# Kernel optimization log

Hardware: AMD Instinct MI355X
Metric: run time of the kernel (lower is better)

The kernel has to match this reference:

```python
import jax, jax.numpy as jnp
import numpy as np

DIM = 1024
HEADS = 16
HIDDEN = 4 * DIM

def _gelu_erf(x):
    # GELU via erf, matching the torch module exactly
    return x * 0.5 * (1.0 + jax.lax.erf(x / jnp.sqrt(2.0).astype(x.dtype)))

def setup_inputs() -> dict:
    key = jax.random.key(0)
    ks = jax.random.split(key, 12)
    s = 0.02
    x = jax.random.normal(ks[0], (2, 2048, DIM), dtype=jnp.float32)
    # MHSA params
    ln1_g = jnp.ones((DIM,), jnp.float32)
    ln1_b = jnp.zeros((DIM,), jnp.float32)
    w_qkv = jax.random.normal(ks[1], (DIM, 3 * DIM), jnp.float32) * s  # no bias
    w_proj = jax.random.normal(ks[2], (DIM, DIM), jnp.float32) * s
    b_proj = jnp.zeros((DIM,), jnp.float32)
    # ResMLP params
    ln2_g = jnp.ones((DIM,), jnp.float32)
    ln2_b = jnp.zeros((DIM,), jnp.float32)
    w1 = jax.random.normal(ks[3], (DIM, HIDDEN), jnp.float32) * s
    b1 = jnp.zeros((HIDDEN,), jnp.float32)
    w2 = jax.random.normal(ks[4], (HIDDEN, DIM), jnp.float32) * s
    b2 = jnp.zeros((DIM,), jnp.float32)
    return {"x": x, "ln1_g": ln1_g, "ln1_b": ln1_b, "w_qkv": w_qkv,
            "w_proj": w_proj, "b_proj": b_proj, "ln2_g": ln2_g, "ln2_b": ln2_b,
            "w1": w1, "b1": b1, "w2": w2, "b2": b2}

def _layernorm(x, g, b, eps=1e-5):
    mu = jnp.mean(x, axis=-1, keepdims=True)
    var = jnp.mean(jnp.square(x - mu), axis=-1, keepdims=True)
    return (x - mu) * jax.lax.rsqrt(var + eps) * g + b

def reference(x, ln1_g, ln1_b, w_qkv, w_proj, b_proj, ln2_g, ln2_b, w1, b1, w2, b2):
    B, N, C = x.shape
    H = HEADS
    hd = C // H
    scale = hd ** -0.5
    # --- MHSA (dropout is identity in eval) ---
    h = _layernorm(x, ln1_g, ln1_b)
    qkv = (h @ w_qkv).reshape(B, N, 3, H, hd)
    q = jnp.transpose(qkv[:, :, 0], (0, 2, 1, 3))  # [B,H,N,hd]
    k = jnp.transpose(qkv[:, :, 1], (0, 2, 1, 3))
    v = jnp.transpose(qkv[:, :, 2], (0, 2, 1, 3))
    attn = jax.nn.softmax(jnp.einsum('bhnd,bhmd->bhnm', q, k) * scale, axis=-1)
    out = jnp.einsum('bhnm,bhmd->bhnd', attn, v)
    out = jnp.transpose(out, (0, 2, 1, 3)).reshape(B, N, C)
    x = x + out @ w_proj + b_proj
    # --- ResMLP ---
    h = _layernorm(x, ln2_g, ln2_b)
    h = _gelu_erf(h @ w1 + b1)
    x = x + h @ w2 + b2
    return x
```

## Files before the change

### kernel.cpp

```cpp
#include <hip/hip_runtime.h>
#include <stdint.h>


#define DIMC 1024
#define HIDN 4096
#define SEQ  2048
#define TOK  4096

typedef __bf16 bf16x8 __attribute__((ext_vector_type(8)));
typedef float  f32x4  __attribute__((ext_vector_type(4)));
typedef unsigned short ushort8 __attribute__((ext_vector_type(8)));

__device__ inline unsigned short f2bf(float f) {
  union { float f; unsigned u; } v; v.f = f;
  unsigned u = v.u;
  return (unsigned short)((u + 0x7fffu + ((u >> 16) & 1u)) >> 16);
}

__device__ inline unsigned cvt_pk_bf16(float a, float b) {
  unsigned r;
  asm("v_cvt_pk_bf16_f32 %0, %1, %2" : "=v"(r) : "v"(a), "v"(b));
  return r;
}

#if __has_builtin(__builtin_amdgcn_exp2f)
__device__ inline float fast_exp2(float x) { return __builtin_amdgcn_exp2f(x); }
#else
__device__ inline float fast_exp2(float x) { return exp2f(x); }
#endif

__device__ inline f32x4 mfma_bf16(bf16x8 a, bf16x8 b, f32x4 c) {
  return __builtin_amdgcn_mfma_f32_16x16x32_bf16(a, b, c, 0, 0, 0);
}

typedef const __attribute__((address_space(1))) unsigned int* as1_u32p;
typedef __attribute__((address_space(3))) unsigned int* as3_u32p;
__device__ inline void gload_lds16(const unsigned short* g, unsigned short* l) {
  __builtin_amdgcn_global_load_lds((as1_u32p)(const void*)g, (as3_u32p)(void*)l,
                                   16, 0, 0);
}

__global__ __launch_bounds__(256)
void prep_kernel(const float* __restrict__ wa, unsigned short* __restrict__ ta,
                 const float* __restrict__ wb, unsigned short* __restrict__ tb,
                 const float* __restrict__ wc, unsigned short* __restrict__ tc,
                 const float* __restrict__ wd, unsigned short* __restrict__ td,
                 const float* __restrict__ x, const float* __restrict__ g,
                 const float* __restrict__ bln, unsigned short* __restrict__ out) {
  const int bid = blockIdx.x;
  const int tid = threadIdx.x;
  if (bid < 12288) {
    __shared__ float tile[32][33];
    const float* w; unsigned short* wt; int K, N, bx, by;
    if (bid < 3072)      { w = wa; wt = ta; K = 1024; N = 3072; bx = bid % 96;  by = bid / 96; }
    else if (bid < 4096) { int i = bid - 3072; w = wb; wt = tb; K = 1024; N = 1024; bx = i % 32;  by = i / 32; }
    else if (bid < 8192) { int i = bid - 4096; w = wc; wt = tc; K = 1024; N = 4096; bx = i % 128; by = i / 128; }
    else                 { int i = bid - 8192; w = wd; wt = td; K = 4096; N = 1024; bx = i % 32;  by = i / 32; }
    const int k0 = by * 32;
    const int n0 = bx * 32;
    const int tx = tid & 31;
    const int ty = tid >> 5;
#pragma unroll
    for (int i = 0; i < 4; i++)
      tile[ty + i * 8][tx] = w[(size_t)(k0 + ty + i * 8) * N + n0 + tx];
    __syncthreads();
#pragma unroll
    for (int i = 0; i < 4; i++)
      wt[(size_t)(n0 + ty + i * 8) * K + k0 + tx] = f2bf(tile[tx][ty + i * 8]);
  } else {
    const int row = bid - 12288;
    const float4* xr = (const float4*)&x[(size_t)row * DIMC];
    float4 v = xr[tid];
    float s  = v.x + v.y + v.z + v.w;
    float sq = v.x * v.x + v.y * v.y + v.z * v.z + v.w * v.w;
#pragma unroll
    for (int off = 32; off > 0; off >>= 1) {
      s  += __shfl_xor(s, off, 64);
      sq += __shfl_xor(sq, off, 64);
    }
    __shared__ float red[8];
    if ((tid & 63) == 0) { red[tid >> 6] = s; red[4 + (tid >> 6)] = sq; }
    __syncthreads();
    s  = red[0] + red[1] + red[2] + red[3];
    sq = red[4] + red[5] + red[6] + red[7];
    const float mu  = s * (1.0f / DIMC);
    const float var = sq * (1.0f / DIMC) - mu * mu;
    const float rs  = rsqrtf(var + 1e-5f);
    const int c = tid * 4;
    float vv[4] = {v.x, v.y, v.z, v.w};
#pragma unroll
    for (int j = 0; j < 4; j++)
      out[(size_t)row * DIMC + c + j] = f2bf((vv[j] - mu) * rs * g[c + j] + bln[c + j]);
  }
}

__global__ __launch_bounds__(256)
void ln_kernel(const float* __restrict__ x, const float* __restrict__ g,
               const float* __restrict__ b, unsigned short* __restrict__ out) {
  const int row = blockIdx.x;
  const int tid = threadIdx.x;
  const float4* xr = (const float4*)&x[(size_t)row * DIMC];
  float4 v = xr[tid];
  float s  = v.x + v.y + v.z + v.w;
  float sq = v.x * v.x + v.y * v.y + v.z * v.z + v.w * v.w;
#pragma unroll
  for (int off = 32; off > 0; off >>= 1) {
    s  += __shfl_xor(s, off, 64);
    sq += __shfl_xor(sq, off, 64);
  }
  __shared__ float red[8];
  if ((tid & 63) == 0) { red[tid >> 6] = s; red[4 + (tid >> 6)] = sq; }
  __syncthreads();
  s  = red[0] + red[1] + red[2] + red[3];
  sq = red[4] + red[5] + red[6] + red[7];
  const float mu  = s * (1.0f / DIMC);
  const float var = sq * (1.0f / DIMC) - mu * mu;
  const float rs  = rsqrtf(var + 1e-5f);
  const int c = tid * 4;
  float vv[4] = {v.x, v.y, v.z, v.w};
#pragma unroll
  for (int j = 0; j < 4; j++)
    out[(size_t)row * DIMC + c + j] = f2bf((vv[j] - mu) * rs * g[c + j] + b[c + j]);
}

template <int EPI, int TN>
__global__ __launch_bounds__(256, (TN == 64) ? 4 : 3)
void gemm_bt(const unsigned short* __restrict__ A,
             const unsigned short* __restrict__ Bt,
             float* __restrict__ Cf, unsigned short* __restrict__ Cb,
             const float* __restrict__ bias, const float* __restrict__ res,
             int M, int N, int K,
             unsigned short* __restrict__ qd,
             unsigned short* __restrict__ kTd,
             unsigned short* __restrict__ vd) {
  constexpr int NU = TN / 32;
  constexpr int BP = TN / 32;
  __shared__ unsigned short As[128 * 64];
  __shared__ unsigned short Bs[TN * 64];
  const int gx  = N / TN;
  const int bid = blockIdx.x;
  const int xcd = bid & 7;
  const int lin = bid >> 3;
  const int bx  = lin % gx;
  const int by  = (xcd << 2) + lin / gx;
  const int tid  = threadIdx.x;
  const int lane = tid & 63;
  const int wave = tid >> 6;
  const int m0 = by * 128;
  const int n0 = bx * TN;
  const int wm = (wave >> 1) * 64;
  const int wn = (wave & 1) * (TN / 2);
  const int lm = lane & 15;
  const int lg = lane >> 4;
  const int r8 = tid >> 3;
  const int c8 = tid & 7;
  const int csrc = ((c8 ^ (r8 & 7)) * 8);

  const unsigned short* gA = &A [(size_t)(m0 + r8) * K + csrc];
  const unsigned short* gB = &Bt[(size_t)(n0 + r8) * K + csrc];

  f32x4 acc[4][NU];
#pragma unroll
  for (int t = 0; t < 4; t++)
#pragma unroll
    for (int u = 0; u < NU; u++) acc[t][u] = {0.f, 0.f, 0.f, 0.f};

  const int x0 = (lg ^ (lm & 7)) * 8;
  const int x1 = ((4 + lg) ^ (lm & 7)) * 8;

  for (int k0 = 0; k0 < K; k0 += 64) {
    __syncthreads();
#pragma unroll
    for (int p = 0; p < 4; p++)
      gload_lds16(gA + (size_t)p * 32 * K + k0, &As[p * 2048 + wave * 512]);
#pragma unroll
    for (int p = 0; p < BP; p++)
      gload_lds16(gB + (size_t)p * 32 * K + k0, &Bs[p * 2048 + wave * 512]);
    __syncthreads();
#pragma unroll
    for (int sub = 0; sub < 2; sub++) {
      const int xo = sub ? x1 : x0;
      bf16x8 af[4], bfr[NU];
#pragma unroll
      for (int t = 0; t < 4; t++)  af[t]  = *(const bf16x8*)&As[(wm + t * 16 + lm) * 64 + xo];
#pragma unroll
      for (int u = 0; u < NU; u++) bfr[u] = *(const bf16x8*)&Bs[(wn + u * 16 + lm) * 64 + xo];
#pragma unroll
      for (int t = 0; t < 4; t++)
#pragma unroll
        for (int u = 0; u < NU; u++)
          acc[t][u] = mfma_bf16(af[t], bfr[u], acc[t][u]);
    }
  }

#pragma unroll
  for (int t = 0; t < 4; t++) {
    const int row = m0 + wm + t * 16 + lg * 4;
#pragma unroll
    for (int u = 0; u < NU; u++) {
      const int col = n0 + wn + u * 16 + lm;
#pragma unroll
      for (int r = 0; r < 4; r++) {
        float v = acc[t][u][r];
        size_t idx = (size_t)(row + r) * N + col;
        if (EPI == 0) {
          const int rr = row + r;
          const int bb = rr >> 11, key = rr & (SEQ - 1);
          if (col < 1024) {
            qd[(size_t)rr * 1024 + col] = f2bf(v * 0.18033688011112042f);
          } else if (col < 2048) {
            const int d = col - 1024, h = d >> 6, dd = d & 63;
            kTd[(((size_t)(bb * 16 + h)) * SEQ + key) * 64 + dd] = f2bf(v);
          } else {
            vd[(size_t)rr * 1024 + (col - 2048)] = f2bf(v);
          }
        } else if (EPI == 1) {
          Cf[idx] = v + bias[col] + res[idx];
        } else {
          float xg = v + bias[col];
          Cb[idx] = f2bf(0.5f * xg * (1.0f + erff(xg * 0.70710678118654752f)));
        }
      }
    }
  }
}

__global__ __launch_bounds__(256)
void v_transpose(const unsigned short* __restrict__ vd,
                 unsigned short* __restrict__ vT) {
  const int kt = blockIdx.x;
  const int bh = blockIdx.y;
  const int b = bh >> 4, h = bh & 15;
  const int tid = threadIdx.x;
  __shared__ unsigned short tile[64 * 72];
  const int tok = tid >> 2;
  const int ch  = tid & 3;
  const size_t srow = (size_t)(b * SEQ + kt * 64 + tok) * 1024 + h * 64;
  ushort8 va = *(const ushort8*)&vd[srow + ch * 8];
  ushort8 vb = *(const ushort8*)&vd[srow + 32 + ch * 8];
  *(ushort8*)&tile[tok * 72 + ch * 8] = va;
  *(ushort8*)&tile[tok * 72 + 32 + ch * 8] = vb;
  __syncthreads();
  const int d = tid >> 2;
  ushort8 o0, o1;
#pragma unroll
  for (int j = 0; j < 8; j++) {
    o0[j] = tile[(ch * 8 + j) * 72 + d];
    o1[j] = tile[((ch + 4) * 8 + j) * 72 + d];
  }
  const size_t vdst = ((size_t)bh * 64 + d) * SEQ + kt * 64;
  *(ushort8*)&vT[vdst + ch * 8] = o0;
  *(ushort8*)&vT[vdst + 32 + ch * 8] = o1;
}

__global__ __launch_bounds__(256, 2)
void attn_kernel(const unsigned short* __restrict__ qbuf,
                 const unsigned short* __restrict__ kT,
                 const unsigned short* __restrict__ vT,
                 unsigned short* __restrict__ out) {
  const int bid = blockIdx.x;
  const int xcd = bid & 7;
  const int lin = bid >> 3;
  const int bh  = (xcd << 2) + (lin >> 4);
  const int qt  = lin & 15;
  const int b  = bh >> 4;
  const int h  = bh & 15;
  const int tid  = threadIdx.x;
  const int lane = tid & 63;
  const int wave = tid >> 6;
  const int ks   = wave >> 1;
  const int qh   = wave & 1;
  const int lm = lane & 15;
  const int lg = lane >> 4;

  __shared__ f32x4 shbuf[4096];
  unsigned short* Ks = (unsigned short*)shbuf;
  unsigned short* Vs = (unsigned short*)shbuf + 8192;
  unsigned short* Ps = (unsigned short*)shbuf + 16384;

  const int qrow_base = b * SEQ + qt * 128 + qh * 64;
  bf16x8 qb[4][2];
#pragma unroll
  for (int s = 0; s < 4; s++)
#pragma unroll
    for (int c = 0; c < 2; c++)
      qb[s][c] = *(const bf16x8*)&qbuf[(size_t)(qrow_base + s * 16 + lm) * 1024 +
                                       h * 64 + c * 32 + lg * 8];

  f32x4 o[4][4];
#pragma unroll
  for (int dt = 0; dt < 4; dt++)
#pragma unroll
    for (int s = 0; s < 4; s++) o[dt][s] = {0.f, 0.f, 0.f, 0.f};
  float li[4] = {0.f, 0.f, 0.f, 0.f};

  const unsigned short* kbp = &kT[(size_t)bh * SEQ * 64];
  const unsigned short* vbp = &vT[(size_t)bh * 64 * SEQ];
  const int ts   = tid & 127;
  const int srow = ts >> 3;
  const int slog = ((ts & 7) ^ (srow & 7)) * 8;
  const int koff = ks * 1024;
  const int xk0 = ((lg)     ^ (lm & 7)) * 8;
  const int xk1 = ((4 + lg) ^ (lm & 7)) * 8;
  unsigned short* ksb = Ks + ks * 4096;
  unsigned short* vsb = Vs + ks * 4096;
  unsigned short* psb = Ps + wave * 4096;
  unsigned short* kdst = ksb + ((ts >> 6) * 512);
  unsigned short* vdst = vsb + ((ts >> 6) * 512);

  for (int kt = 0; kt < 16; kt++) {
    __syncthreads();
#pragma unroll
    for (int p = 0; p < 4; p++) {
      gload_lds16(&kbp[(size_t)(koff + kt * 64 + p * 16 + srow) * 64 + slog],
                  kdst + p * 1024);
      gload_lds16(&vbp[(size_t)(p * 16 + srow) * SEQ + koff + kt * 64 + slog],
                  vdst + p * 1024);
    }
    __syncthreads();

#pragma unroll
    for (int u = 0; u < 4; u++) {
      bf16x8 ka0 = *(const bf16x8*)&ksb[(u * 16 + lm) * 64 + xk0];
      bf16x8 ka1 = *(const bf16x8*)&ksb[(u * 16 + lm) * 64 + xk1];
      f32x4 st[4];
#pragma unroll
      for (int s = 0; s < 4; s++) {
        f32x4 z = {0.f, 0.f, 0.f, 0.f};
        z = mfma_bf16(ka0, qb[s][0], z);
        z = mfma_bf16(ka1, qb[s][1], z);
        st[s] = z;
      }
#pragma unroll
      for (int s = 0; s < 4; s++) {
        float p0 = fast_exp2(st[s][0] - 8.0f);
        float p1 = fast_exp2(st[s][1] - 8.0f);
        float p2 = fast_exp2(st[s][2] - 8.0f);
        float p3 = fast_exp2(st[s][3] - 8.0f);
        li[s] += (p0 + p1) + (p2 + p3);
        uint2 pk;
        pk.x = cvt_pk_bf16(p0, p1);
        pk.y = cvt_pk_bf16(p2, p3);
        const int phys = (u * 2 + (lg >> 1)) ^ (lm & 7);
        *(uint2*)&psb[(s * 16 + lm) * 64 + phys * 8 + (lg & 1) * 4] = pk;
      }
    }

#pragma unroll
    for (int kc = 0; kc < 2; kc++) {
      const int xo = kc ? xk1 : xk0;
      bf16x8 pb[4];
#pragma unroll
      for (int s = 0; s < 4; s++)
        pb[s] = *(const bf16x8*)&psb[(s * 16 + lm) * 64 + xo];
#pragma unroll
      for (int dt = 0; dt < 4; dt++) {
        bf16x8 va = *(const bf16x8*)&vsb[(dt * 16 + lm) * 64 + xo];
#pragma unroll
        for (int s = 0; s < 4; s++)
          o[dt][s] = mfma_bf16(va, pb[s], o[dt][s]);
      }
    }
  }

  __syncthreads();
  f32x4* ob = shbuf + qh * 1088;
  float*  lb = (float*)(ob + 1024);
  if (ks == 1) {
#pragma unroll
    for (int dt = 0; dt < 4; dt++)
#pragma unroll
      for (int s = 0; s < 4; s++)
        ob[(dt * 4 + s) * 64 + lane] = o[dt][s];
#pragma unroll
    for (int s = 0; s < 4; s++) lb[s * 64 + lane] = li[s];
  }
  __syncthreads();
  if (ks == 0) {
#pragma unroll
    for (int dt = 0; dt < 4; dt++)
#pragma unroll
      for (int s = 0; s < 4; s++)
        o[dt][s] += ob[(dt * 4 + s) * 64 + lane];
#pragma unroll
    for (int s = 0; s < 4; s++) {
      float l = li[s] + lb[s * 64 + lane];
      l += __shfl_xor(l, 16, 64);
      l += __shfl_xor(l, 32, 64);
      const float inv = 1.0f / l;
#pragma unroll
      for (int dt = 0; dt < 4; dt++) {
        uint2 ok;
        ok.x = cvt_pk_bf16(o[dt][s][0] * inv, o[dt][s][1] * inv);
        ok.y = cvt_pk_bf16(o[dt][s][2] * inv, o[dt][s][3] * inv);
        *(uint2*)&out[(size_t)(qrow_base + s * 16 + lm) * DIMC + h * 64 +
                      dt * 16 + lg * 4] = ok;
      }
    }
  }
}

extern "C" void kernel_launch(void* const* d_in, const int* in_sizes, int n_in,
                              void* d_out, int out_size, void* d_ws, size_t ws_size,
                              hipStream_t stream) {
  const float* x      = (const float*)d_in[0];
  const float* ln1_g  = (const float*)d_in[1];
  const float* ln1_b  = (const float*)d_in[2];
  const float* w_qkv  = (const float*)d_in[3];
  const float* w_proj = (const float*)d_in[4];
  const float* b_proj = (const float*)d_in[5];
  const float* ln2_g  = (const float*)d_in[6];
  const float* ln2_b  = (const float*)d_in[7];
  const float* w1     = (const float*)d_in[8];
  const float* b1     = (const float*)d_in[9];
  const float* w2     = (const float*)d_in[10];
  const float* b2     = (const float*)d_in[11];
  float* out = (float*)d_out;

  char* ws = (char*)d_ws;
  size_t off = 0;
  auto alloc = [&](size_t bytes) { void* p = ws + off; off += (bytes + 255) & ~(size_t)255; return p; };
  unsigned short* wqkvT = (unsigned short*)alloc((size_t)3072 * 1024 * 2);
  unsigned short* wprjT = (unsigned short*)alloc((size_t)1024 * 1024 * 2);
  unsigned short* w1T   = (unsigned short*)alloc((size_t)4096 * 1024 * 2);
  unsigned short* w2T   = (unsigned short*)alloc((size_t)1024 * 4096 * 2);
  unsigned short* hb    = (unsigned short*)alloc((size_t)TOK * 1024 * 2);
  unsigned short* qbuf  = (unsigned short*)alloc((size_t)TOK * 1024 * 2);
  unsigned short* vdb   = (unsigned short*)alloc((size_t)TOK * 1024 * 2);
  unsigned short* attnb = (unsigned short*)alloc((size_t)TOK * 1024 * 2);
  float*          x1    = (float*)         alloc((size_t)TOK * 1024 * 4);
  unsigned short* hidb  = (unsigned short*)alloc((size_t)TOK * 4096 * 2);
  unsigned short* kT = hidb;
  unsigned short* vT = hidb + (size_t)32 * SEQ * 64;

  prep_kernel<<<12288 + TOK, 256, 0, stream>>>(w_qkv, wqkvT, w_proj, wprjT,
                                               w1, w1T, w2, w2T,
                                               x, ln1_g, ln1_b, hb);
  gemm_bt<0, 64><<<1536, 256, 0, stream>>>(
      hb, wqkvT, nullptr, nullptr, nullptr, nullptr, TOK, 3072, 1024,
      qbuf, kT, vdb);
  v_transpose<<<dim3(SEQ / 64, 32), 256, 0, stream>>>(vdb, vT);
  attn_kernel<<<512, 256, 0, stream>>>(qbuf, kT, vT, attnb);
  gemm_bt<1, 64><<<512, 256, 0, stream>>>(
      attnb, wprjT, x1, nullptr, b_proj, x, TOK, 1024, 1024,
      nullptr, nullptr, nullptr);
  ln_kernel<<<TOK, 256, 0, stream>>>(x1, ln2_g, ln2_b, hb);
  gemm_bt<2, 64><<<2048, 256, 0, stream>>>(
      hb, w1T, nullptr, hidb, b1, nullptr, TOK, 4096, 1024,
      nullptr, nullptr, nullptr);
  gemm_bt<1, 64><<<512, 256, 0, stream>>>(
      hidb, w2T, out, nullptr, b2, x1, TOK, 1024, 4096,
      nullptr, nullptr, nullptr);
}
```

Measured before the change: 339.6 us.

## Double-buffer LDS tiles in gemm_bt to overlap global loads with MFMA

```diff
diff --git a/kernel.cpp b/kernel.cpp
--- a/kernel.cpp
+++ b/kernel.cpp
@@ -124,7 +124,7 @@
 }
 
 template <int EPI, int TN>
-__global__ __launch_bounds__(256, (TN == 64) ? 4 : 3)
+__global__ __launch_bounds__(256, 3)
 void gemm_bt(const unsigned short* __restrict__ A,
              const unsigned short* __restrict__ Bt,
              float* __restrict__ Cf, unsigned short* __restrict__ Cb,
@@ -135,8 +135,10 @@
              unsigned short* __restrict__ vd) {
   constexpr int NU = TN / 32;
   constexpr int BP = TN / 32;
-  __shared__ unsigned short As[128 * 64];
-  __shared__ unsigned short Bs[TN * 64];
+  __shared__ unsigned short As0[128 * 64];
+  __shared__ unsigned short Bs0[TN * 64];
+  __shared__ unsigned short As1[128 * 64];
+  __shared__ unsigned short Bs1[TN * 64];
   const int gx  = N / TN;
   const int bid = blockIdx.x;
   const int xcd = bid & 7;
@@ -168,30 +170,55 @@
   const int x0 = (lg ^ (lm & 7)) * 8;
   const int x1 = ((4 + lg) ^ (lm & 7)) * 8;
 
-  for (int k0 = 0; k0 < K; k0 += 64) {
-    __syncthreads();
-#pragma unroll
-    for (int p = 0; p < 4; p++)
-      gload_lds16(gA + (size_t)p * 32 * K + k0, &As[p * 2048 + wave * 512]);
-#pragma unroll
-    for (int p = 0; p < BP; p++)
-      gload_lds16(gB + (size_t)p * 32 * K + k0, &Bs[p * 2048 + wave * 512]);
-    __syncthreads();
-#pragma unroll
-    for (int sub = 0; sub < 2; sub++) {
-      const int xo = sub ? x1 : x0;
-      bf16x8 af[4], bfr[NU];
-#pragma unroll
-      for (int t = 0; t < 4; t++)  af[t]  = *(const bf16x8*)&As[(wm + t * 16 + lm) * 64 + xo];
-#pragma unroll
-      for (int u = 0; u < NU; u++) bfr[u] = *(const bf16x8*)&Bs[(wn + u * 16 + lm) * 64 + xo];
-#pragma unroll
-      for (int t = 0; t < 4; t++)
-#pragma unroll
-        for (int u = 0; u < NU; u++)
-          acc[t][u] = mfma_bf16(af[t], bfr[u], acc[t][u]);
-    }
-  }
+#define STG_T(ABUF, BBUF, KO)                                                  \
+  do {                                                                         \
+    _Pragma("unroll")                                                          \
+    for (int p = 0; p < 4; p++)                                                \
+      gload_lds16(gA + (size_t)p * 32 * K + (KO), &ABUF[p * 2048 + wave * 512]); \
+    _Pragma("unroll")                                                          \
+    for (int p = 0; p < BP; p++)                                               \
+      gload_lds16(gB + (size_t)p * 32 * K + (KO), &BBUF[p * 2048 + wave * 512]); \
+  } while (0)
+
+#define CMP_T(ABUF, BBUF)                                                      \
+  do {                                                                         \
+    _Pragma("unroll")                                                          \
+    for (int sub = 0; sub < 2; sub++) {                                        \
+      const int xo = sub ? x1 : x0;                                            \
+      bf16x8 af[4], bfr[NU];                                                   \
+      _Pragma("unroll")                                                        \
+      for (int t = 0; t < 4; t++)                                              \
+        af[t] = *(const bf16x8*)&ABUF[(wm + t * 16 + lm) * 64 + xo];           \
+      _Pragma("unroll")                                                        \
+      for (int u = 0; u < NU; u++)                                             \
+        bfr[u] = *(const bf16x8*)&BBUF[(wn + u * 16 + lm) * 64 + xo];          \
+      _Pragma("unroll")                                                        \
+      for (int t = 0; t < 4; t++)                                              \
+        _Pragma("unroll")                                                      \
+        for (int u = 0; u < NU; u++)                                           \
+          acc[t][u] = mfma_bf16(af[t], bfr[u], acc[t][u]);                     \
+    }                                                                          \
+  } while (0)
+
+  STG_T(As0, Bs0, 0);
+  __syncthreads();
+
+#pragma unroll 1
+  for (int k0 = 0; k0 + 128 < K; k0 += 128) {
+    STG_T(As1, Bs1, k0 + 64);
+    CMP_T(As0, Bs0);
+    __syncthreads();
+    STG_T(As0, Bs0, k0 + 128);
+    CMP_T(As1, Bs1);
+    __syncthreads();
+  }
+  STG_T(As1, Bs1, K - 64);
+  CMP_T(As0, Bs0);
+  __syncthreads();
+  CMP_T(As1, Bs1);
+
+#undef STG_T
+#undef CMP_T
 
 #pragma unroll
   for (int t = 0; t < 4; t++) {
```

Result: no change. 341.2 us (+0.5%).
